# Kernel tuning notes

Measured on AMD Instinct MI355X. Metric: run time of the kernel, lower is better.

Reference implementation:

```python
import jax, jax.numpy as jnp
import numpy as np

B, N1, N2 = 16, 196, 196
C1, C2, H, O = 768, 768, 512, 128


def setup_inputs() -> dict:
    key = jax.random.key(0)
    k1, k2, kw1, kw2, kwp, kbp = jax.random.split(key, 6)
    x1 = jax.random.normal(k1, (B, N1, C1), dtype=jnp.float32)
    x2 = jax.random.normal(k2, (B, N2, C2), dtype=jnp.float32)
    # kaiming-uniform-ish init scale
    W1 = jax.random.uniform(kw1, (C1, H), dtype=jnp.float32, minval=-1, maxval=1) * np.sqrt(3.0 / C1)
    W2 = jax.random.uniform(kw2, (C2, H), dtype=jnp.float32, minval=-1, maxval=1) * np.sqrt(3.0 / C2)
    Wp = jax.random.uniform(kwp, (H, O), dtype=jnp.float32, minval=-1, maxval=1) * np.sqrt(3.0 / H)
    bp = jax.random.uniform(kbp, (O,), dtype=jnp.float32, minval=-1, maxval=1) * (1.0 / np.sqrt(H))
    return {"x1": x1, "x2": x2, "W1": W1, "W2": W2, "Wp": Wp, "bp": bp}


def reference(x1, x2, W1, W2, Wp, bp):
    # x1: [B,N1,C1], x2: [B,N2,C2]
    h1 = jax.nn.relu(jnp.einsum('bnc,ch->bnh', x1, W1))  # [B,N1,H]
    h2 = jax.nn.relu(jnp.einsum('bmc,ch->bmh', x2, W2))  # [B,N2,H]
    # Original: ((h1[:,:,None,:] * h2[:,None,:,:]) @ Wp + bp).sum(dim=(1,2)).
    # Mathematically identical fused form: sum_{i,j} h1[b,i,h]*h2[b,j,h]
    #   = (sum_i h1)[b,h] * (sum_j h2)[b,h]; bias accumulates N1*N2 times.
    s = h1.sum(axis=1) * h2.sum(axis=1)                   # [B,H]
    return jnp.einsum('bh,ho->bo', s, Wp) + bp * (N1 * N2)
```

## Files before the change

### kernel.cpp

```cpp
#include <hip/hip_runtime.h>
#include <hip/hip_bf16.h>


#define NB 16
#define NROW 196
#define KC_ 768
#define HH 512
#define OO 128

using short8 = __attribute__((ext_vector_type(8))) short;
using f32x16 = __attribute__((ext_vector_type(16))) float;

__device__ __forceinline__ short2 pk2bf(float a, float b) {
    __hip_bfloat162 h = __float22bfloat162_rn(make_float2(a, b));
    union { __hip_bfloat162 h; short2 s; } u; u.h = h;
    return u.s;
}

__global__ __launch_bounds__(256)
void w_tile(const float* __restrict__ W1, const float* __restrict__ W2,
            unsigned short* __restrict__ Wt) {
    const int t = threadIdx.x;
    const int bb = blockIdx.x;
    const int branch = bb / 48;
    const int rem = bb % 48;
    const int ht = rem / 12;
    const int kc = rem % 12;
    const float* __restrict__ W = branch ? W2 : W1;
    unsigned short* __restrict__ out = Wt + (size_t)bb * 8192;
#pragma unroll
    for (int i = 0; i < 4; ++i) {
        const int u = i * 256 + t;
        const int p = u >> 7, col = u & 127;
        const float* src = W + (kc * 64 + p * 8) * HH + ht * 128 + col;
        float f[8];
#pragma unroll
        for (int j = 0; j < 8; ++j) f[j] = src[j * HH];
        short8 v; short2 s;
#pragma unroll
        for (int j = 0; j < 4; ++j) {
            s = pk2bf(f[2 * j], f[2 * j + 1]); v[2 * j] = s.x; v[2 * j + 1] = s.y;
        }
        *(short8*)(out + u * 8) = v;
    }
}

__global__ __launch_bounds__(256, 2)
void gemm_relu_rowsum(const float* __restrict__ x1, const float* __restrict__ x2,
                      const unsigned short* __restrict__ Wt,
                      float* __restrict__ sbuf) {
    __shared__ unsigned short Alds[2][8 * 64 * 8];
    __shared__ unsigned short Blds[2][8 * 128 * 8];
    __shared__ float psum[8 * 32];

    const int bid = blockIdx.x;
    const int p  = bid & 31;
    const int tt = bid >> 5;
    const int branch = p >> 4;
    const int b      = p & 15;
    const int ht = tt >> 2;
    const int mq = tt & 3;

    const float* __restrict__ x = branch ? x2 : x1;
    const unsigned short* __restrict__ Wtb = Wt + (size_t)((branch * 4 + ht) * 12) * 8192;

    const int t    = threadIdx.x;
    const int row  = t >> 2;
    const int slot = t & 3;
    const int r_abs = mq * 64 + row;
    const bool valid = r_abs < NROW;
    const float* xrow = x + (b * NROW + (valid ? r_abs : 0)) * KC_ + slot * 16;

    float4 av[4];
    short8 bv[4];

    auto load_stage = [&](int kc) {
        if (valid) {
#pragma unroll
            for (int i = 0; i < 4; ++i)
                av[i] = *(const float4*)(xrow + kc * 64 + 4 * i);
        } else {
#pragma unroll
            for (int i = 0; i < 4; ++i) av[i] = make_float4(0.f, 0.f, 0.f, 0.f);
        }
        const unsigned short* wc = Wtb + kc * 8192;
#pragma unroll
        for (int i = 0; i < 4; ++i)
            bv[i] = *(const short8*)(wc + (t + 256 * i) * 8);
    };

    auto write_stage = [&](int buf) {
        short8 v0, v1; short2 s;
        s = pk2bf(av[0].x, av[0].y); v0[0] = s.x; v0[1] = s.y;
        s = pk2bf(av[0].z, av[0].w); v0[2] = s.x; v0[3] = s.y;
        s = pk2bf(av[1].x, av[1].y); v0[4] = s.x; v0[5] = s.y;
        s = pk2bf(av[1].z, av[1].w); v0[6] = s.x; v0[7] = s.y;
        s = pk2bf(av[2].x, av[2].y); v1[0] = s.x; v1[1] = s.y;
        s = pk2bf(av[2].z, av[2].w); v1[2] = s.x; v1[3] = s.y;
        s = pk2bf(av[3].x, av[3].y); v1[4] = s.x; v1[5] = s.y;
        s = pk2bf(av[3].z, av[3].w); v1[6] = s.x; v1[7] = s.y;
        *(short8*)&Alds[buf][((slot * 2 + 0) * 64 + row) * 8] = v0;
        *(short8*)&Alds[buf][((slot * 2 + 1) * 64 + row) * 8] = v1;
#pragma unroll
        for (int i = 0; i < 4; ++i)
            *(short8*)&Blds[buf][(t + 256 * i) * 8] = bv[i];
    };

    const int w  = t >> 6;
    const int l  = t & 63;
    const int m  = l & 31;
    const int q  = l >> 5;
    const int sp = w & 1;
    const int mp = w >> 1;
    const int aoff = (mp * 32 + m) * 8;
    const int boff = (sp * 64 + m) * 8;

    f32x16 acc0 = {}, acc1 = {};

    load_stage(0);
    write_stage(0);
    load_stage(1);
    __syncthreads();

#pragma unroll 1
    for (int kc = 0; kc < 12; ++kc) {
        const int pb = kc & 1;
#pragma unroll
        for (int ks = 0; ks < 4; ++ks) {
            const int kp = ks * 2 + q;
            short8 af = *(const short8*)&Alds[pb][kp * 512 + aoff];
            short8 b0 = *(const short8*)&Blds[pb][kp * 1024 + boff];
            short8 b1 = *(const short8*)&Blds[pb][kp * 1024 + boff + 256];
            acc0 = __builtin_amdgcn_mfma_f32_32x32x16_bf16(af, b0, acc0, 0, 0, 0);
            acc1 = __builtin_amdgcn_mfma_f32_32x32x16_bf16(af, b1, acc1, 0, 0, 0);
        }
        if (kc < 11) write_stage(1 - pb);
        if (kc < 10) load_stage(kc + 2);
        __syncthreads();
    }

    float cs0 = 0.f, cs1 = 0.f;
#pragma unroll
    for (int r = 0; r < 16; ++r) {
        cs0 += fmaxf(acc0[r], 0.f);
        cs1 += fmaxf(acc1[r], 0.f);
    }
    cs0 += __shfl_xor(cs0, 32);
    cs1 += __shfl_xor(cs1, 32);
    if (l < 32) {
        psum[((sp * 2 + 0) * 2 + mp) * 32 + l] = cs0;
        psum[((sp * 2 + 1) * 2 + mp) * 32 + l] = cs1;
    }
    __syncthreads();
    if (t < 128) {
        const int ct = t >> 5;
        const int cl = t & 31;
        const float v = psum[(ct * 2 + 0) * 32 + cl] + psum[(ct * 2 + 1) * 32 + cl];
        sbuf[((branch * 4 + mq) * NB + b) * HH + ht * 128 + t] = v;
    }
}

__global__ __launch_bounds__(512)
void proj_kernel(const float* __restrict__ sbuf, const float* __restrict__ Wp,
                 const float* __restrict__ bp, float* __restrict__ out) {
    __shared__ float spl[HH];
    __shared__ float red[4][OO];
    const int b = blockIdx.x, t = threadIdx.x;
    {
        float s1 = 0.f, s2 = 0.f;
#pragma unroll
        for (int i = 0; i < 4; ++i) {
            s1 += sbuf[((0 + i) * NB + b) * HH + t];
            s2 += sbuf[((4 + i) * NB + b) * HH + t];
        }
        spl[t] = s1 * s2;
    }
    __syncthreads();
    const int to = t & 127, hq = t >> 7;
    float acc = 0.f;
#pragma unroll 8
    for (int h = hq * 128; h < hq * 128 + 128; ++h)
        acc += spl[h] * Wp[h * OO + to];
    red[hq][to] = acc;
    __syncthreads();
    if (t < OO)
        out[b * OO + t] = red[0][t] + red[1][t] + red[2][t] + red[3][t]
                        + bp[t] * 38416.0f;
}

extern "C" void kernel_launch(void* const* d_in, const int* in_sizes, int n_in,
                              void* d_out, int out_size, void* d_ws, size_t ws_size,
                              hipStream_t stream) {
    const float* x1 = (const float*)d_in[0];
    const float* x2 = (const float*)d_in[1];
    const float* W1 = (const float*)d_in[2];
    const float* W2 = (const float*)d_in[3];
    const float* Wp = (const float*)d_in[4];
    const float* bp = (const float*)d_in[5];
    float* sbuf = (float*)d_ws;
    unsigned short* Wt = (unsigned short*)((char*)d_ws + 262144);

    w_tile<<<96, 256, 0, stream>>>(W1, W2, Wt);
    gemm_relu_rowsum<<<512, 256, 0, stream>>>(x1, x2, Wt, sbuf);
    proj_kernel<<<NB, 512, 0, stream>>>(sbuf, Wp, bp, (float*)d_out);
}
```

Baseline: 95.12 us.

## Load GEMM fragments directly from global into registers, dropping LDS staging

The GEMM kernel no longer stages A and B tiles through double-buffered shared memory with barriers. Each lane now loads its MFMA fragments straight from global memory into registers, double-buffered across k-chunks, and converts x to bf16 just before each MFMA. The pre-tiled weight layout is reordered to match the per-lane fragment pattern, and out-of-range rows read from a zeroed row in workspace. This removes LDS traffic and __syncthreads, but each wave now loads its own copy of data that was previously shared across waves, raising global/L2 traffic and register pressure.

```diff
diff --git a/kernel.cpp b/kernel.cpp
--- a/kernel.cpp
+++ b/kernel.cpp
@@ -19,9 +19,12 @@
 
 __global__ __launch_bounds__(256)
 void w_tile(const float* __restrict__ W1, const float* __restrict__ W2,
-            unsigned short* __restrict__ Wt) {
+            unsigned short* __restrict__ Wt, float* __restrict__ zrow) {
     const int t = threadIdx.x;
     const int bb = blockIdx.x;
+    if (bb == 0) {
+        zrow[t] = 0.f; zrow[t + 256] = 0.f; zrow[t + 512] = 0.f;
+    }
     const int branch = bb / 48;
     const int rem = bb % 48;
     const int ht = rem / 12;
@@ -31,8 +34,11 @@
 #pragma unroll
     for (int i = 0; i < 4; ++i) {
         const int u = i * 256 + t;
-        const int p = u >> 7, col = u & 127;
-        const float* src = W + (kc * 64 + p * 8) * HH + ht * 128 + col;
+        const int m  = u & 31;
+        const int a  = (u >> 5) & 1;
+        const int sp = (u >> 6) & 1;
+        const int kp = u >> 7;
+        const float* src = W + (kc * 64 + kp * 8) * HH + ht * 128 + sp * 64 + a * 32 + m;
         float f[8];
 #pragma unroll
         for (int j = 0; j < 8; ++j) f[j] = src[j * HH];
@@ -48,9 +54,8 @@
 __global__ __launch_bounds__(256, 2)
 void gemm_relu_rowsum(const float* __restrict__ x1, const float* __restrict__ x2,
                       const unsigned short* __restrict__ Wt,
+                      const float* __restrict__ zrow,
                       float* __restrict__ sbuf) {
-    __shared__ unsigned short Alds[2][8 * 64 * 8];
-    __shared__ unsigned short Blds[2][8 * 128 * 8];
     __shared__ float psum[8 * 32];
 
     const int bid = blockIdx.x;
@@ -64,79 +69,55 @@
     const float* __restrict__ x = branch ? x2 : x1;
     const unsigned short* __restrict__ Wtb = Wt + (size_t)((branch * 4 + ht) * 12) * 8192;
 
-    const int t    = threadIdx.x;
-    const int row  = t >> 2;
-    const int slot = t & 3;
-    const int r_abs = mq * 64 + row;
-    const bool valid = r_abs < NROW;
-    const float* xrow = x + (b * NROW + (valid ? r_abs : 0)) * KC_ + slot * 16;
-
-    float4 av[4];
-    short8 bv[4];
-
-    auto load_stage = [&](int kc) {
-        if (valid) {
-#pragma unroll
-            for (int i = 0; i < 4; ++i)
-                av[i] = *(const float4*)(xrow + kc * 64 + 4 * i);
-        } else {
-#pragma unroll
-            for (int i = 0; i < 4; ++i) av[i] = make_float4(0.f, 0.f, 0.f, 0.f);
-        }
-        const unsigned short* wc = Wtb + kc * 8192;
-#pragma unroll
-        for (int i = 0; i < 4; ++i)
-            bv[i] = *(const short8*)(wc + (t + 256 * i) * 8);
-    };
-
-    auto write_stage = [&](int buf) {
-        short8 v0, v1; short2 s;
-        s = pk2bf(av[0].x, av[0].y); v0[0] = s.x; v0[1] = s.y;
-        s = pk2bf(av[0].z, av[0].w); v0[2] = s.x; v0[3] = s.y;
-        s = pk2bf(av[1].x, av[1].y); v0[4] = s.x; v0[5] = s.y;
-        s = pk2bf(av[1].z, av[1].w); v0[6] = s.x; v0[7] = s.y;
-        s = pk2bf(av[2].x, av[2].y); v1[0] = s.x; v1[1] = s.y;
-        s = pk2bf(av[2].z, av[2].w); v1[2] = s.x; v1[3] = s.y;
-        s = pk2bf(av[3].x, av[3].y); v1[4] = s.x; v1[5] = s.y;
-        s = pk2bf(av[3].z, av[3].w); v1[6] = s.x; v1[7] = s.y;
-        *(short8*)&Alds[buf][((slot * 2 + 0) * 64 + row) * 8] = v0;
-        *(short8*)&Alds[buf][((slot * 2 + 1) * 64 + row) * 8] = v1;
-#pragma unroll
-        for (int i = 0; i < 4; ++i)
-            *(short8*)&Blds[buf][(t + 256 * i) * 8] = bv[i];
-    };
-
+    const int t  = threadIdx.x;
     const int w  = t >> 6;
     const int l  = t & 63;
     const int m  = l & 31;
     const int q  = l >> 5;
     const int sp = w & 1;
     const int mp = w >> 1;
-    const int aoff = (mp * 32 + m) * 8;
-    const int boff = (sp * 64 + m) * 8;
+
+    const int r_abs = mq * 64 + mp * 32 + m;
+    const float* xrow = (r_abs < NROW) ? (x + (size_t)(b * NROW + r_abs) * KC_) : zrow;
+
+    auto load_frag = [&](float4 (&fa)[8], short8 (&fb)[8], int kc) {
+        const float* xp = xrow + kc * 64;
+        const unsigned short* wp = Wtb + kc * 8192;
+#pragma unroll
+        for (int ks = 0; ks < 4; ++ks) {
+            const int kp = ks * 2 + q;
+            fa[2 * ks]     = *(const float4*)(xp + kp * 8);
+            fa[2 * ks + 1] = *(const float4*)(xp + kp * 8 + 4);
+            const unsigned short* bp_ = wp + ((kp * 2 + sp) * 2) * 256 + m * 8;
+            fb[2 * ks]     = *(const short8*)(bp_);
+            fb[2 * ks + 1] = *(const short8*)(bp_ + 256);
+        }
+    };
 
     f32x16 acc0 = {}, acc1 = {};
 
-    load_stage(0);
-    write_stage(0);
-    load_stage(1);
-    __syncthreads();
-
-#pragma unroll 1
-    for (int kc = 0; kc < 12; ++kc) {
-        const int pb = kc & 1;
+    auto compute = [&](const float4 (&fa)[8], const short8 (&fb)[8]) {
 #pragma unroll
         for (int ks = 0; ks < 4; ++ks) {
-            const int kp = ks * 2 + q;
-            short8 af = *(const short8*)&Alds[pb][kp * 512 + aoff];
-            short8 b0 = *(const short8*)&Blds[pb][kp * 1024 + boff];
-            short8 b1 = *(const short8*)&Blds[pb][kp * 1024 + boff + 256];
-            acc0 = __builtin_amdgcn_mfma_f32_32x32x16_bf16(af, b0, acc0, 0, 0, 0);
-            acc1 = __builtin_amdgcn_mfma_f32_32x32x16_bf16(af, b1, acc1, 0, 0, 0);
+            const float4 lo = fa[2 * ks], hi = fa[2 * ks + 1];
+            short8 af; short2 s;
+            s = pk2bf(lo.x, lo.y); af[0] = s.x; af[1] = s.y;
+            s = pk2bf(lo.z, lo.w); af[2] = s.x; af[3] = s.y;
+            s = pk2bf(hi.x, hi.y); af[4] = s.x; af[5] = s.y;
+            s = pk2bf(hi.z, hi.w); af[6] = s.x; af[7] = s.y;
+            acc0 = __builtin_amdgcn_mfma_f32_32x32x16_bf16(af, fb[2 * ks],     acc0, 0, 0, 0);
+            acc1 = __builtin_amdgcn_mfma_f32_32x32x16_bf16(af, fb[2 * ks + 1], acc1, 0, 0, 0);
         }
-        if (kc < 11) write_stage(1 - pb);
-        if (kc < 10) load_stage(kc + 2);
-        __syncthreads();
+    };
+
+    float4 a0[8], a1[8]; short8 b0f[8], b1f[8];
+    load_frag(a0, b0f, 0);
+#pragma unroll 1
+    for (int j = 0; j < 6; ++j) {
+        load_frag(a1, b1f, 2 * j + 1);
+        compute(a0, b0f);
+        if (j < 5) load_frag(a0, b0f, 2 * j + 2);
+        compute(a1, b1f);
     }
 
     float cs0 = 0.f, cs1 = 0.f;
@@ -199,8 +180,9 @@
     const float* bp = (const float*)d_in[5];
     float* sbuf = (float*)d_ws;
     unsigned short* Wt = (unsigned short*)((char*)d_ws + 262144);
+    float* zrow = (float*)((char*)d_ws + 262144 + 1572864);
 
-    w_tile<<<96, 256, 0, stream>>>(W1, W2, Wt);
-    gemm_relu_rowsum<<<512, 256, 0, stream>>>(x1, x2, Wt, sbuf);
+    w_tile<<<96, 256, 0, stream>>>(W1, W2, Wt, zrow);
+    gemm_relu_rowsum<<<512, 256, 0, stream>>>(x1, x2, Wt, zrow, sbuf);
     proj_kernel<<<NB, 512, 0, stream>>>(sbuf, Wp, bp, (float*)d_out);
 }
```

Measured after the change: 108.9 us. +14.5%, slower.
